# Kernel optimization log

Hardware: AMD Instinct MI355X
Metric: run time of the kernel (lower is better)

The kernel has to match this reference:

```python
import jax, jax.numpy as jnp
import numpy as np
import math

D_MODEL = 1024
N_HEADS = 16
HEAD_DIM = D_MODEL // N_HEADS
SEQ = 2048
BATCH = 4
MAX_SEQ_LEN = 2048
THETA = 10000.0


def setup_inputs() -> dict:
    key = jax.random.key(0)
    ks = jax.random.split(key, 5)
    std = math.sqrt(2.0 / (D_MODEL + D_MODEL))
    x = jax.random.normal(ks[0], (BATCH, SEQ, D_MODEL), dtype=jnp.float32)
    wq = jax.random.normal(ks[1], (D_MODEL, D_MODEL), dtype=jnp.float32) * std
    wk = jax.random.normal(ks[2], (D_MODEL, D_MODEL), dtype=jnp.float32) * std
    wv = jax.random.normal(ks[3], (D_MODEL, D_MODEL), dtype=jnp.float32) * std
    wo = jax.random.normal(ks[4], (D_MODEL, D_MODEL), dtype=jnp.float32) * std
    token_positions = jnp.arange(SEQ, dtype=jnp.int32)
    return {"x": x, "token_positions": token_positions,
            "wq": wq, "wk": wk, "wv": wv, "wo": wo}


def _rope_tables(token_positions):
    # thetas_i = 1 / theta^(2i/d_k), angles[p, i] = p * thetas_i
    thetas = 1.0 / (THETA ** (2.0 * jnp.arange(HEAD_DIM // 2, dtype=jnp.float32) / HEAD_DIM))
    positions = jnp.arange(MAX_SEQ_LEN, dtype=jnp.float32)
    angles = jnp.outer(positions, thetas)  # [max_seq, d_k/2]
    cos = jnp.cos(angles)[token_positions]  # [S, d_k/2]
    sin = jnp.sin(angles)[token_positions]
    return cos, sin


def _apply_rope(x, cos, sin):
    # x: [B, H, S, D]; pairs (even, odd) form complex numbers
    shp = x.shape
    x2 = x.reshape(*shp[:-1], HEAD_DIM // 2, 2)
    xe, xo = x2[..., 0], x2[..., 1]
    re = xe * cos - xo * sin
    im = xe * sin + xo * cos
    return jnp.stack([re, im], axis=-1).reshape(shp)


def reference(x, token_positions, wq, wk, wv, wo):
    B, S, _ = x.shape
    # LinearNoBias: einsum('...j,ij->...i', x, W)
    q = jnp.einsum('bsj,ij->bsi', x, wq)
    k = jnp.einsum('bsj,ij->bsi', x, wk)
    v = jnp.einsum('bsj,ij->bsi', x, wv)
    # split heads -> [B, H, S, D]
    q = q.reshape(B, S, N_HEADS, HEAD_DIM).transpose(0, 2, 1, 3)
    k = k.reshape(B, S, N_HEADS, HEAD_DIM).transpose(0, 2, 1, 3)
    v = v.reshape(B, S, N_HEADS, HEAD_DIM).transpose(0, 2, 1, 3)
    cos, sin = _rope_tables(token_positions)
    q = _apply_rope(q, cos, sin)
    k = _apply_rope(k, cos, sin)
    scores = jnp.einsum('bhqd,bhkd->bhqk', q, k) / math.sqrt(HEAD_DIM)
    causal = jnp.tril(jnp.ones((S, S), dtype=bool))
    scores = jnp.where(causal, scores, -jnp.inf)
    probs = jax.nn.softmax(scores, axis=-1)
    out = jnp.einsum('bhqk,bhkd->bhqd', probs, v)
    out = out.transpose(0, 2, 1, 3).reshape(B, S, N_HEADS * HEAD_DIM)
    return jnp.einsum('bsj,ij->bsi', out, wo)
```

## Files before the change

### kernel.cpp

```cpp
#include <hip/hip_runtime.h>
#include <stdint.h>

#define B_SZ 4
#define S_LEN 2048
#define NH 16
#define HD 64
#define DM 1024

typedef __bf16 bf16;
typedef __bf16 bf16x4 __attribute__((ext_vector_type(4)));
typedef __bf16 bf16x8 __attribute__((ext_vector_type(8)));
typedef float f32x4 __attribute__((ext_vector_type(4)));

#define MFMA16(a, b, c) __builtin_amdgcn_mfma_f32_16x16x32_bf16(a, b, c, 0, 0, 0)

__device__ __forceinline__ bf16x8 ldcvt(const float* p) {
  f32x4 u0 = *(const f32x4*)p;
  f32x4 u1 = *(const f32x4*)(p + 4);
  bf16x8 v;
#pragma unroll
  for (int j = 0; j < 4; j++) {
    v[j] = (bf16)u0[j];
    v[4 + j] = (bf16)u1[j];
  }
  return v;
}

#define GP 40
template <bool AF32, bool BF32>
__device__ __forceinline__ void gemm_core(const void* Agv, const void* Bgv,
                                          f32x4 acc[4][4], bf16* As, bf16* Bs) {
  const float* Af = (const float*)Agv;
  const bf16* Ab = (const bf16*)Agv;
  const float* Bf = (const float*)Bgv;
  const bf16* Bb = (const bf16*)Bgv;
  const int tid = threadIdx.x;
  const int lane = tid & 63;
  const int wave = tid >> 6;
  const int wm = (wave >> 1) * 64;
  const int wn = (wave & 1) * 64;
  const int col = lane & 15;
  const int kq = (lane >> 4) * 8;
  const int r0 = tid >> 2;
  const int c0 = (tid & 3) * 8;
#pragma unroll
  for (int i = 0; i < 4; i++)
#pragma unroll
    for (int j = 0; j < 4; j++) acc[i][j] = (f32x4){0.f, 0.f, 0.f, 0.f};

  for (int k0 = 0; k0 < 1024; k0 += 32) {
    bf16x8 a0, a1, b0, b1;
    if (AF32) {
      a0 = ldcvt(Af + (size_t)r0 * 1024 + k0 + c0);
      a1 = ldcvt(Af + (size_t)(r0 + 64) * 1024 + k0 + c0);
    } else {
      a0 = *(const bf16x8*)(Ab + (size_t)r0 * 1024 + k0 + c0);
      a1 = *(const bf16x8*)(Ab + (size_t)(r0 + 64) * 1024 + k0 + c0);
    }
    if (BF32) {
      b0 = ldcvt(Bf + (size_t)r0 * 1024 + k0 + c0);
      b1 = ldcvt(Bf + (size_t)(r0 + 64) * 1024 + k0 + c0);
    } else {
      b0 = *(const bf16x8*)(Bb + (size_t)r0 * 1024 + k0 + c0);
      b1 = *(const bf16x8*)(Bb + (size_t)(r0 + 64) * 1024 + k0 + c0);
    }
    __syncthreads();
    *(bf16x8*)(As + r0 * GP + c0) = a0;
    *(bf16x8*)(As + (r0 + 64) * GP + c0) = a1;
    *(bf16x8*)(Bs + r0 * GP + c0) = b0;
    *(bf16x8*)(Bs + (r0 + 64) * GP + c0) = b1;
    __syncthreads();

    bf16x8 af[4], bfr[4];
#pragma unroll
    for (int i = 0; i < 4; i++)
      af[i] = *(const bf16x8*)(As + (wm + i * 16 + col) * GP + kq);
#pragma unroll
    for (int j = 0; j < 4; j++)
      bfr[j] = *(const bf16x8*)(Bs + (wn + j * 16 + col) * GP + kq);
#pragma unroll
    for (int i = 0; i < 4; i++)
#pragma unroll
      for (int j = 0; j < 4; j++)
        acc[i][j] = MFMA16(af[i], bfr[j], acc[i][j]);
  }
}

__global__ __launch_bounds__(256, 2) void qkv_gemm(
    const float* __restrict__ x, const float* __restrict__ wq,
    const float* __restrict__ wk, const float* __restrict__ wv,
    bf16* __restrict__ ws, size_t ten_stride) {
  __shared__ __align__(16) bf16 As[128 * GP];
  __shared__ __align__(16) bf16 Bs[128 * GP];
  const int bx = blockIdx.x;
  const int by = blockIdx.y;
  const int wsel = by >> 3;
  const int n0 = (by & 7) * 128;
  const float* W = (wsel == 0) ? wq : ((wsel == 1) ? wk : wv);
  bf16* dst = ws + (size_t)wsel * ten_stride;

  f32x4 acc[4][4];
  gemm_core<true, true>(x + (size_t)bx * 128 * 1024, W + (size_t)n0 * 1024,
                        acc, As, Bs);

  const int lane = threadIdx.x & 63;
  const int wave = threadIdx.x >> 6;
  const int wm = (wave >> 1) * 64, wn = (wave & 1) * 64;
  const int col = lane & 15, quad = lane >> 4;
#pragma unroll
  for (int i = 0; i < 4; i++) {
    const int m0 = bx * 128 + wm + i * 16 + quad * 4;
#pragma unroll
    for (int j = 0; j < 4; j++) {
      const int n = n0 + wn + j * 16 + col;
      const int h = n >> 6, d = n & 63;
#pragma unroll
      for (int r = 0; r < 4; r++) {
        const int mm = m0 + r;
        const int bl = mm >> 11, s = mm & 2047;
        dst[((((size_t)bl * NH + h) * S_LEN + s) << 6) + d] = (bf16)acc[i][j][r];
      }
    }
  }
}

__global__ void rope_kernel(bf16* __restrict__ q, bf16* __restrict__ k,
                            const int* __restrict__ tp) {
  const int idx = blockIdx.x * 256 + threadIdx.x;
  const int srow = idx >> 3;
  const int d0 = (idx & 7) * 8;
  const int s = srow & (S_LEN - 1);
  const float pf = (float)tp[s];
  const int i0 = d0 >> 1;
  float cs[4], sn[4];
#pragma unroll
  for (int j = 0; j < 4; j++) {
    float freq = __builtin_exp2f(-(float)(i0 + j) * 0.41524101186091903f);
    float ang = pf * freq;
    sincosf(ang, &sn[j], &cs[j]);
  }
  const size_t off = (size_t)srow * 64 + d0;
  bf16x8 vq = *(bf16x8*)(q + off);
  bf16x8 vk = *(bf16x8*)(k + off);
#pragma unroll
  for (int j = 0; j < 4; j++) {
    float e = (float)vq[2 * j], o = (float)vq[2 * j + 1];
    vq[2 * j] = (bf16)(e * cs[j] - o * sn[j]);
    vq[2 * j + 1] = (bf16)(e * sn[j] + o * cs[j]);
    e = (float)vk[2 * j];
    o = (float)vk[2 * j + 1];
    vk[2 * j] = (bf16)(e * cs[j] - o * sn[j]);
    vk[2 * j + 1] = (bf16)(e * sn[j] + o * cs[j]);
  }
  *(bf16x8*)(q + off) = vq;
  *(bf16x8*)(k + off) = vk;
}

__global__ void transpose_v(const bf16* __restrict__ v, bf16* __restrict__ vt) {
  __shared__ __align__(16) bf16 t[64 * 72];
  const int st = blockIdx.x, bh = blockIdx.y;
  const bf16* src = v + ((size_t)bh * S_LEN + st * 64) * 64;
#pragma unroll
  for (int p = 0; p < 2; p++) {
    int g = p * 256 + threadIdx.x;
    int r = g >> 3, c = (g & 7) * 8;
    bf16x8 val = *(const bf16x8*)(src + r * 64 + c);
#pragma unroll
    for (int j = 0; j < 8; j++) t[(c + j) * 72 + r] = val[j];
  }
  __syncthreads();
  bf16* dst = vt + (size_t)bh * 64 * S_LEN + st * 64;
#pragma unroll
  for (int p = 0; p < 2; p++) {
    int g = p * 256 + threadIdx.x;
    int d = g >> 3, sc = (g & 7) * 8;
    *(bf16x8*)(dst + (size_t)d * S_LEN + sc) = *(const bf16x8*)(t + d * 72 + sc);
  }
}

#define KP 72
#define VP 136
#define PP 72
__global__ __launch_bounds__(256, 2) void attn_kernel(
    const bf16* __restrict__ Q, const bf16* __restrict__ K,
    const bf16* __restrict__ Vt, bf16* __restrict__ O) {
  __shared__ __align__(16) bf16 Ks[128 * KP];
  __shared__ __align__(16) bf16 Vts[64 * VP];
  __shared__ __align__(16) bf16 Ps[4 * 32 * PP];

  const int tid = threadIdx.x, lane = tid & 63, wave = tid >> 6;
  const int col = lane & 15, quad = lane >> 4, kq = quad * 8;
  const int bh = blockIdx.y;
  const int bl = bh >> 4, h = bh & 15;
  const bf16* Kg = K + (size_t)bh * S_LEN * 64;
  const bf16* Vg = Vt + (size_t)bh * 64 * S_LEN;
  bf16* Pw = Ps + wave * 32 * PP;
  const int wq0 = wave * 32;
  const float CS = 0.18033688011112042f;

  for (int half = 0; half < 2; half++) {
    const int qt = half ? (int)blockIdx.x : 15 - (int)blockIdx.x;
    const bf16* Qg = Q + ((size_t)bh * S_LEN + qt * 128) * 64;
    bf16x8 qf[2][2];
#pragma unroll
    for (int mi = 0; mi < 2; mi++)
#pragma unroll
      for (int kc = 0; kc < 2; kc++)
        qf[mi][kc] =
            *(const bf16x8*)(Qg + (wq0 + mi * 16 + col) * 64 + kc * 32 + kq);

    f32x4 oacc[2][4];
    float mst[2] = {-1e30f, -1e30f}, lst[2] = {0.f, 0.f};
#pragma unroll
    for (int mi = 0; mi < 2; mi++)
#pragma unroll
      for (int nd = 0; nd < 4; nd++) oacc[mi][nd] = (f32x4){0.f, 0.f, 0.f, 0.f};

    for (int kt = 0; kt <= qt; kt++) {
      bf16x8 kreg[4], vreg[4];
#pragma unroll
      for (int p = 0; p < 4; p++) {
        int g = p * 256 + tid;
        kreg[p] = *(const bf16x8*)(Kg + (size_t)(kt * 128 + (g >> 3)) * 64 +
                                   (g & 7) * 8);
        vreg[p] = *(const bf16x8*)(Vg + (size_t)(g >> 4) * S_LEN + kt * 128 +
                                   (g & 15) * 8);
      }
      __syncthreads();
#pragma unroll
      for (int p = 0; p < 4; p++) {
        int g = p * 256 + tid;
        *(bf16x8*)(Ks + (g >> 3) * KP + (g & 7) * 8) = kreg[p];
        *(bf16x8*)(Vts + (g >> 4) * VP + (g & 15) * 8) = vreg[p];
      }
      __syncthreads();

      f32x4 sa[2][8];
#pragma unroll
      for (int ni = 0; ni < 8; ni++) {
        bf16x8 kf0 = *(const bf16x8*)(Ks + (ni * 16 + col) * KP + kq);
        bf16x8 kf1 = *(const bf16x8*)(Ks + (ni * 16 + col) * KP + 32 + kq);
#pragma unroll
        for (int mi = 0; mi < 2; mi++) {
          f32x4 s = {0.f, 0.f, 0.f, 0.f};
          s = MFMA16(kf0, qf[mi][0], s);
          s = MFMA16(kf1, qf[mi][1], s);
          sa[mi][ni] = s;
        }
      }
      if (kt == qt) {
#pragma unroll
        for (int mi = 0; mi < 2; mi++) {
          const int qloc = wq0 + mi * 16 + col;
#pragma unroll
          for (int ni = 0; ni < 8; ni++)
#pragma unroll
            for (int r = 0; r < 4; r++)
              if (ni * 16 + quad * 4 + r > qloc) sa[mi][ni][r] = -1e30f;
        }
      }
#pragma unroll
      for (int mi = 0; mi < 2; mi++) {
        float mx = sa[mi][0][0];
#pragma unroll
        for (int ni = 0; ni < 8; ni++)
#pragma unroll
          for (int r = 0; r < 4; r++) mx = fmaxf(mx, sa[mi][ni][r]);
        mx = fmaxf(mx, __shfl_xor(mx, 16));
        mx = fmaxf(mx, __shfl_xor(mx, 32));
        const float mnew = fmaxf(mst[mi], mx);
        const float alpha = __builtin_exp2f((mst[mi] - mnew) * CS);
        mst[mi] = mnew;
        float rs = 0.f;
#pragma unroll
        for (int ni = 0; ni < 8; ni++)
#pragma unroll
          for (int r = 0; r < 4; r++) {
            float pv = __builtin_exp2f((sa[mi][ni][r] - mnew) * CS);
            sa[mi][ni][r] = pv;
            rs += pv;
          }
        rs += __shfl_xor(rs, 16);
        rs += __shfl_xor(rs, 32);
        lst[mi] = lst[mi] * alpha + rs;
        float av[4];
#pragma unroll
        for (int r = 0; r < 4; r++) av[r] = __shfl(alpha, quad * 4 + r);
#pragma unroll
        for (int nd = 0; nd < 4; nd++)
#pragma unroll
          for (int r = 0; r < 4; r++) oacc[mi][nd][r] *= av[r];
      }
#pragma unroll
      for (int hf = 0; hf < 2; hf++) {
#pragma unroll
        for (int mi = 0; mi < 2; mi++)
#pragma unroll
          for (int nn = 0; nn < 4; nn++) {
            const int ni = hf * 4 + nn;
            bf16x4 pk;
#pragma unroll
            for (int r = 0; r < 4; r++) pk[r] = (bf16)sa[mi][ni][r];
            *(bf16x4*)(Pw + (mi * 16 + col) * PP + nn * 16 + quad * 4) = pk;
          }
#pragma unroll
        for (int kcl = 0; kcl < 2; kcl++) {
          const int kc = hf * 2 + kcl;
          bf16x8 pf0 = *(const bf16x8*)(Pw + col * PP + kcl * 32 + kq);
          bf16x8 pf1 = *(const bf16x8*)(Pw + (16 + col) * PP + kcl * 32 + kq);
#pragma unroll
          for (int nd = 0; nd < 4; nd++) {
            bf16x8 vf =
                *(const bf16x8*)(Vts + (nd * 16 + col) * VP + kc * 32 + kq);
            oacc[0][nd] = MFMA16(pf0, vf, oacc[0][nd]);
            oacc[1][nd] = MFMA16(pf1, vf, oacc[1][nd]);
          }
        }
      }
    }

#pragma unroll
    for (int mi = 0; mi < 2; mi++) {
      const float il = 1.0f / lst[mi];
      float linv[4];
#pragma unroll
      for (int r = 0; r < 4; r++) linv[r] = __shfl(il, quad * 4 + r);
      const int srow0 = qt * 128 + wq0 + mi * 16 + quad * 4;
#pragma unroll
      for (int nd = 0; nd < 4; nd++)
#pragma unroll
        for (int r = 0; r < 4; r++)
          O[(size_t)(bl * S_LEN + srow0 + r) * DM + h * 64 + nd * 16 + col] =
              (bf16)(oacc[mi][nd][r] * linv[r]);
    }
  }
}

__global__ __launch_bounds__(256, 2) void out_gemm(const bf16* __restrict__ A,
                                                   const float* __restrict__ W,
                                                   float* __restrict__ out) {
  __shared__ __align__(16) bf16 As[128 * GP];
  __shared__ __align__(16) bf16 Bs[128 * GP];
  f32x4 acc[4][4];
  gemm_core<false, true>(A + (size_t)blockIdx.x * 128 * 1024,
                         W + (size_t)blockIdx.y * 128 * 1024, acc, As, Bs);
  const int lane = threadIdx.x & 63;
  const int wave = threadIdx.x >> 6;
  const int wm = (wave >> 1) * 64, wn = (wave & 1) * 64;
  const int col = lane & 15, quad = lane >> 4;
#pragma unroll
  for (int i = 0; i < 4; i++) {
    const int m0 = blockIdx.x * 128 + wm + i * 16 + quad * 4;
#pragma unroll
    for (int j = 0; j < 4; j++) {
      const int n = blockIdx.y * 128 + wn + j * 16 + col;
#pragma unroll
      for (int r = 0; r < 4; r++)
        out[(size_t)(m0 + r) * DM + n] = acc[i][j][r];
    }
  }
}

extern "C" void kernel_launch(void* const* d_in, const int* in_sizes, int n_in,
                              void* d_out, int out_size, void* d_ws,
                              size_t ws_size, hipStream_t stream) {
  const float* x = (const float*)d_in[0];
  const int* tp = (const int*)d_in[1];
  const float* wq = (const float*)d_in[2];
  const float* wk = (const float*)d_in[3];
  const float* wv = (const float*)d_in[4];
  const float* wo = (const float*)d_in[5];
  float* out = (float*)d_out;
  bf16* wsb = (bf16*)d_ws;

  const size_t TENb = (size_t)NH * S_LEN * HD;
  int bcnt = 1;
  if (ws_size >= 4 * 4 * TENb * sizeof(bf16)) bcnt = 4;
  else if (ws_size >= 2 * 4 * TENb * sizeof(bf16)) bcnt = 2;

  const size_t REG = (size_t)bcnt * TENb;
  bf16* Qw = wsb;
  bf16* Kw = wsb + REG;
  bf16* Vw = wsb + 2 * REG;
  bf16* Vtw = wsb + 3 * REG;
  bf16* Ow = Vw;

  for (int b0 = 0; b0 < B_SZ; b0 += bcnt) {
    const float* xb = x + (size_t)b0 * S_LEN * DM;
    float* outb = out + (size_t)b0 * S_LEN * DM;
    hipLaunchKernelGGL(qkv_gemm, dim3(bcnt * 16, 24), dim3(256), 0, stream,
                       xb, wq, wk, wv, Qw, REG);
    hipLaunchKernelGGL(rope_kernel, dim3(bcnt * 1024), dim3(256), 0, stream,
                       Qw, Kw, tp);
    hipLaunchKernelGGL(transpose_v, dim3(32, bcnt * 16), dim3(256), 0, stream,
                       Vw, Vtw);
    hipLaunchKernelGGL(attn_kernel, dim3(8, bcnt * 16), dim3(256), 0, stream,
                       Qw, Kw, Vtw, Ow);
    hipLaunchKernelGGL(out_gemm, dim3(bcnt * 16, 8), dim3(256), 0, stream,
                       Ow, wo, outb);
  }
}
```

Measured before the change: 308.0 us.

## Pre-convert inputs to bf16, use direct global-to-LDS loads, write V transposed

Adds a conversion kernel that turns x and all four weight matrices into bf16 in the workspace. Both GEMMs can then load tiles straight into LDS with global_load_lds instead of staging through registers, and they drop the padding in LDS. The QKV GEMM writes V directly in transposed layout, which removes the separate transpose kernel, and the launch bounds are raised to 4 blocks per CU. In exchange there is an extra full pass over x and the weights on every call, and the unpadded LDS layout may cause bank conflicts when fragments are read.

```diff
diff --git a/kernel.cpp b/kernel.cpp
--- a/kernel.cpp
+++ b/kernel.cpp
@@ -14,6 +14,12 @@
 
 #define MFMA16(a, b, c) __builtin_amdgcn_mfma_f32_16x16x32_bf16(a, b, c, 0, 0, 0)
 
+__device__ __forceinline__ void gl2lds16(const void* g, void* l) {
+  __builtin_amdgcn_global_load_lds(
+      (__attribute__((address_space(1))) const void*)g,
+      (__attribute__((address_space(3))) void*)l, 16, 0, 0);
+}
+
 __device__ __forceinline__ bf16x8 ldcvt(const float* p) {
   f32x4 u0 = *(const f32x4*)p;
   f32x4 u1 = *(const f32x4*)(p + 4);
@@ -26,14 +32,33 @@
   return v;
 }
 
-#define GP 40
-template <bool AF32, bool BF32>
-__device__ __forceinline__ void gemm_core(const void* Agv, const void* Bgv,
-                                          f32x4 acc[4][4], bf16* As, bf16* Bs) {
-  const float* Af = (const float*)Agv;
-  const bf16* Ab = (const bf16*)Agv;
-  const float* Bf = (const float*)Bgv;
-  const bf16* Bb = (const bf16*)Bgv;
+__global__ void cvt_kernel(const float* __restrict__ x,
+                           const float* __restrict__ wq,
+                           const float* __restrict__ wk,
+                           const float* __restrict__ wv,
+                           const float* __restrict__ wo,
+                           bf16* __restrict__ Xb, bf16* __restrict__ Wb,
+                           long xN) {
+  const long e = ((long)blockIdx.x * 256 + threadIdx.x) * 8;
+  const float* src;
+  bf16* dst;
+  long off;
+  if (e < xN) {
+    src = x; dst = Xb; off = e;
+  } else {
+    const long w = e - xN;
+    const int wi = (int)(w >> 20);
+    src = (wi == 0) ? wq : (wi == 1) ? wk : (wi == 2) ? wv : wo;
+    dst = Wb + ((size_t)wi << 20);
+    off = w & ((1L << 20) - 1);
+  }
+  *(bf16x8*)(dst + off) = ldcvt(src + off);
+}
+
+__device__ __forceinline__ void gemm_core_bb(const bf16* __restrict__ Ag,
+                                             const bf16* __restrict__ Bg,
+                                             f32x4 acc[4][4], bf16* As,
+                                             bf16* Bs) {
   const int tid = threadIdx.x;
   const int lane = tid & 63;
   const int wave = tid >> 6;
@@ -49,35 +74,20 @@
     for (int j = 0; j < 4; j++) acc[i][j] = (f32x4){0.f, 0.f, 0.f, 0.f};
 
   for (int k0 = 0; k0 < 1024; k0 += 32) {
-    bf16x8 a0, a1, b0, b1;
-    if (AF32) {
-      a0 = ldcvt(Af + (size_t)r0 * 1024 + k0 + c0);
-      a1 = ldcvt(Af + (size_t)(r0 + 64) * 1024 + k0 + c0);
-    } else {
-      a0 = *(const bf16x8*)(Ab + (size_t)r0 * 1024 + k0 + c0);
-      a1 = *(const bf16x8*)(Ab + (size_t)(r0 + 64) * 1024 + k0 + c0);
-    }
-    if (BF32) {
-      b0 = ldcvt(Bf + (size_t)r0 * 1024 + k0 + c0);
-      b1 = ldcvt(Bf + (size_t)(r0 + 64) * 1024 + k0 + c0);
-    } else {
-      b0 = *(const bf16x8*)(Bb + (size_t)r0 * 1024 + k0 + c0);
-      b1 = *(const bf16x8*)(Bb + (size_t)(r0 + 64) * 1024 + k0 + c0);
-    }
     __syncthreads();
-    *(bf16x8*)(As + r0 * GP + c0) = a0;
-    *(bf16x8*)(As + (r0 + 64) * GP + c0) = a1;
-    *(bf16x8*)(Bs + r0 * GP + c0) = b0;
-    *(bf16x8*)(Bs + (r0 + 64) * GP + c0) = b1;
+    gl2lds16(Ag + (size_t)r0 * 1024 + k0 + c0, As + tid * 8);
+    gl2lds16(Ag + (size_t)(r0 + 64) * 1024 + k0 + c0, As + 2048 + tid * 8);
+    gl2lds16(Bg + (size_t)r0 * 1024 + k0 + c0, Bs + tid * 8);
+    gl2lds16(Bg + (size_t)(r0 + 64) * 1024 + k0 + c0, Bs + 2048 + tid * 8);
     __syncthreads();
 
     bf16x8 af[4], bfr[4];
 #pragma unroll
     for (int i = 0; i < 4; i++)
-      af[i] = *(const bf16x8*)(As + (wm + i * 16 + col) * GP + kq);
+      af[i] = *(const bf16x8*)(As + (wm + i * 16 + col) * 32 + kq);
 #pragma unroll
     for (int j = 0; j < 4; j++)
-      bfr[j] = *(const bf16x8*)(Bs + (wn + j * 16 + col) * GP + kq);
+      bfr[j] = *(const bf16x8*)(Bs + (wn + j * 16 + col) * 32 + kq);
 #pragma unroll
     for (int i = 0; i < 4; i++)
 #pragma unroll
@@ -86,39 +96,56 @@
   }
 }
 
-__global__ __launch_bounds__(256, 2) void qkv_gemm(
-    const float* __restrict__ x, const float* __restrict__ wq,
-    const float* __restrict__ wk, const float* __restrict__ wv,
-    bf16* __restrict__ ws, size_t ten_stride) {
-  __shared__ __align__(16) bf16 As[128 * GP];
-  __shared__ __align__(16) bf16 Bs[128 * GP];
+__global__ __launch_bounds__(256, 4) void qkv_gemm(
+    const bf16* __restrict__ x, const bf16* __restrict__ Wb,
+    bf16* __restrict__ Q, bf16* __restrict__ K, bf16* __restrict__ Vt) {
+  __shared__ __align__(16) bf16 As[128 * 32];
+  __shared__ __align__(16) bf16 Bs[128 * 32];
   const int bx = blockIdx.x;
   const int by = blockIdx.y;
   const int wsel = by >> 3;
   const int n0 = (by & 7) * 128;
-  const float* W = (wsel == 0) ? wq : ((wsel == 1) ? wk : wv);
-  bf16* dst = ws + (size_t)wsel * ten_stride;
 
   f32x4 acc[4][4];
-  gemm_core<true, true>(x + (size_t)bx * 128 * 1024, W + (size_t)n0 * 1024,
-                        acc, As, Bs);
+  gemm_core_bb(x + (size_t)bx * 128 * 1024,
+               Wb + ((size_t)wsel << 20) + (size_t)n0 * 1024, acc, As, Bs);
 
   const int lane = threadIdx.x & 63;
   const int wave = threadIdx.x >> 6;
   const int wm = (wave >> 1) * 64, wn = (wave & 1) * 64;
   const int col = lane & 15, quad = lane >> 4;
-#pragma unroll
-  for (int i = 0; i < 4; i++) {
-    const int m0 = bx * 128 + wm + i * 16 + quad * 4;
-#pragma unroll
-    for (int j = 0; j < 4; j++) {
-      const int n = n0 + wn + j * 16 + col;
-      const int h = n >> 6, d = n & 63;
-#pragma unroll
-      for (int r = 0; r < 4; r++) {
-        const int mm = m0 + r;
-        const int bl = mm >> 11, s = mm & 2047;
-        dst[((((size_t)bl * NH + h) * S_LEN + s) << 6) + d] = (bf16)acc[i][j][r];
+
+  if (wsel < 2) {
+    bf16* dst = wsel ? K : Q;
+#pragma unroll
+    for (int i = 0; i < 4; i++) {
+      const int m0 = bx * 128 + wm + i * 16 + quad * 4;
+#pragma unroll
+      for (int j = 0; j < 4; j++) {
+        const int n = n0 + wn + j * 16 + col;
+        const int h = n >> 6, d = n & 63;
+#pragma unroll
+        for (int r = 0; r < 4; r++) {
+          const int mm = m0 + r;
+          const int bl = mm >> 11, s = mm & 2047;
+          dst[((((size_t)bl * NH + h) * S_LEN + s) << 6) + d] =
+              (bf16)acc[i][j][r];
+        }
+      }
+    }
+  } else {
+#pragma unroll
+    for (int i = 0; i < 4; i++) {
+      const int m0 = bx * 128 + wm + i * 16 + quad * 4;
+      const int bl = m0 >> 11, s = m0 & 2047;
+#pragma unroll
+      for (int j = 0; j < 4; j++) {
+        const int n = n0 + wn + j * 16 + col;
+        const int h = n >> 6, d = n & 63;
+        bf16x4 pk;
+#pragma unroll
+        for (int r = 0; r < 4; r++) pk[r] = (bf16)acc[i][j][r];
+        *(bf16x4*)(Vt + (((size_t)(bl * NH + h) * 64 + d) << 11) + s) = pk;
       }
     }
   }
@@ -156,28 +183,6 @@
   *(bf16x8*)(k + off) = vk;
 }
 
-__global__ void transpose_v(const bf16* __restrict__ v, bf16* __restrict__ vt) {
-  __shared__ __align__(16) bf16 t[64 * 72];
-  const int st = blockIdx.x, bh = blockIdx.y;
-  const bf16* src = v + ((size_t)bh * S_LEN + st * 64) * 64;
-#pragma unroll
-  for (int p = 0; p < 2; p++) {
-    int g = p * 256 + threadIdx.x;
-    int r = g >> 3, c = (g & 7) * 8;
-    bf16x8 val = *(const bf16x8*)(src + r * 64 + c);
-#pragma unroll
-    for (int j = 0; j < 8; j++) t[(c + j) * 72 + r] = val[j];
-  }
-  __syncthreads();
-  bf16* dst = vt + (size_t)bh * 64 * S_LEN + st * 64;
-#pragma unroll
-  for (int p = 0; p < 2; p++) {
-    int g = p * 256 + threadIdx.x;
-    int d = g >> 3, sc = (g & 7) * 8;
-    *(bf16x8*)(dst + (size_t)d * S_LEN + sc) = *(const bf16x8*)(t + d * 72 + sc);
-  }
-}
-
 #define KP 72
 #define VP 136
 #define PP 72
@@ -336,14 +341,14 @@
   }
 }
 
-__global__ __launch_bounds__(256, 2) void out_gemm(const bf16* __restrict__ A,
-                                                   const float* __restrict__ W,
+__global__ __launch_bounds__(256, 4) void out_gemm(const bf16* __restrict__ A,
+                                                   const bf16* __restrict__ W,
                                                    float* __restrict__ out) {
-  __shared__ __align__(16) bf16 As[128 * GP];
-  __shared__ __align__(16) bf16 Bs[128 * GP];
+  __shared__ __align__(16) bf16 As[128 * 32];
+  __shared__ __align__(16) bf16 Bs[128 * 32];
   f32x4 acc[4][4];
-  gemm_core<false, true>(A + (size_t)blockIdx.x * 128 * 1024,
-                         W + (size_t)blockIdx.y * 128 * 1024, acc, As, Bs);
+  gemm_core_bb(A + (size_t)blockIdx.x * 128 * 1024,
+               W + (size_t)blockIdx.y * 128 * 1024, acc, As, Bs);
   const int lane = threadIdx.x & 63;
   const int wave = threadIdx.x >> 6;
   const int wm = (wave >> 1) * 64, wn = (wave & 1) * 64;
@@ -374,29 +379,32 @@
   bf16* wsb = (bf16*)d_ws;
 
   const size_t TENb = (size_t)NH * S_LEN * HD;
+  const size_t WSZ = 4ull * DM * DM;
   int bcnt = 1;
-  if (ws_size >= 4 * 4 * TENb * sizeof(bf16)) bcnt = 4;
-  else if (ws_size >= 2 * 4 * TENb * sizeof(bf16)) bcnt = 2;
+  if (ws_size >= (4 * 4 * TENb + WSZ) * sizeof(bf16)) bcnt = 4;
+  else if (ws_size >= (4 * 2 * TENb + WSZ) * sizeof(bf16)) bcnt = 2;
 
   const size_t REG = (size_t)bcnt * TENb;
-  bf16* Qw = wsb;
-  bf16* Kw = wsb + REG;
-  bf16* Vw = wsb + 2 * REG;
+  bf16* Xb = wsb;
+  bf16* Qw = wsb + REG;
+  bf16* Kw = wsb + 2 * REG;
   bf16* Vtw = wsb + 3 * REG;
-  bf16* Ow = Vw;
+  bf16* Wb = wsb + 4 * REG;
+  bf16* Ow = Xb;
 
   for (int b0 = 0; b0 < B_SZ; b0 += bcnt) {
     const float* xb = x + (size_t)b0 * S_LEN * DM;
     float* outb = out + (size_t)b0 * S_LEN * DM;
+    const long cvtN = (long)(REG + WSZ);
+    hipLaunchKernelGGL(cvt_kernel, dim3((unsigned)(cvtN / 2048)), dim3(256), 0,
+                       stream, xb, wq, wk, wv, wo, Xb, Wb, (long)REG);
     hipLaunchKernelGGL(qkv_gemm, dim3(bcnt * 16, 24), dim3(256), 0, stream,
-                       xb, wq, wk, wv, Qw, REG);
+                       Xb, Wb, Qw, Kw, Vtw);
     hipLaunchKernelGGL(rope_kernel, dim3(bcnt * 1024), dim3(256), 0, stream,
                        Qw, Kw, tp);
-    hipLaunchKernelGGL(transpose_v, dim3(32, bcnt * 16), dim3(256), 0, stream,
-                       Vw, Vtw);
     hipLaunchKernelGGL(attn_kernel, dim3(8, bcnt * 16), dim3(256), 0, stream,
                        Qw, Kw, Vtw, Ow);
     hipLaunchKernelGGL(out_gemm, dim3(bcnt * 16, 8), dim3(256), 0, stream,
-                       Ow, wo, outb);
-  }
-}
+                       Ow, Wb + 3ull * DM * DM, outb);
+  }
+}
```

New measurement: 279.1 us. 1.1x faster.
